# Kernel optimization log

Measured on AMD Instinct MI355X. Metric: run time of the kernel, lower is better.

## Reference

```python
import jax, jax.numpy as jnp
import numpy as np

N = 100_000      # nodes
E = 1_600_000    # edges (no self loops; reference appends them)
G = 1_000        # graphs
FIN = 27         # input node features
HID = 128        # hidden_channels
L = 4            # num_layers
H = 8            # num_heads
B = 4            # num_bases
A = 3            # aggregators: sum, mean, max
FH = HID // H    # per-head out dim
EPS = 1e-5


def setup_inputs() -> dict:
    key = jax.random.key(0)
    ks = jax.random.split(key, 16)
    s = 0.05
    x = jax.random.normal(ks[0], (N, FIN), jnp.float32)
    src = jax.random.randint(ks[1], (E,), 0, N)
    off = jax.random.randint(ks[2], (E,), 1, N)
    dst = (src + off) % N  # guaranteed no self loops
    edge_index = jnp.stack([src, dst]).astype(jnp.int64)
    batch = jnp.sort(jax.random.randint(ks[3], (N,), 0, G)).astype(jnp.int64)
    return {
        "x": x,
        "lin1_w": jax.random.normal(ks[4], (FIN, HID), jnp.float32) * s,
        "lin1_b": jnp.zeros((HID,), jnp.float32),
        "bn1_g": jnp.ones((HID,), jnp.float32),
        "bn1_b": jnp.zeros((HID,), jnp.float32),
        "bases_w": jax.random.normal(ks[5], (L, HID, B * FH), jnp.float32) * s,
        "comb_w": jax.random.normal(ks[6], (L, HID, H * B * A), jnp.float32) * s,
        "comb_b": jnp.zeros((L, H * B * A), jnp.float32),
        "conv_bias": jnp.zeros((L, HID), jnp.float32),
        "bn_g": jnp.ones((L, HID), jnp.float32),
        "bn_b": jnp.zeros((L, HID), jnp.float32),
        "mlp_w1": jax.random.normal(ks[7], (HID, HID // 2), jnp.float32) * s,
        "mbn1_g": jnp.ones((HID // 2,), jnp.float32),
        "mbn1_b": jnp.zeros((HID // 2,), jnp.float32),
        "mlp_w2": jax.random.normal(ks[8], (HID // 2, HID // 4), jnp.float32) * s,
        "mbn2_g": jnp.ones((HID // 4,), jnp.float32),
        "mbn2_b": jnp.zeros((HID // 4,), jnp.float32),
        "mlp_w3": jax.random.normal(ks[9], (HID // 4, 10), jnp.float32) * s,
        "mlp_b3": jnp.zeros((10,), jnp.float32),
        "edge_index": edge_index,
        "batch": batch,
    }


def _bn(h, g, b):
    # BatchNorm1d, training mode (biased batch variance), per-feature over nodes
    mu = jnp.mean(h, axis=0)
    var = jnp.mean((h - mu) ** 2, axis=0)
    return g * (h - mu) * jax.lax.rsqrt(var + EPS) + b


def reference(x, lin1_w, lin1_b, bn1_g, bn1_b, bases_w, comb_w, comb_b,
              conv_bias, bn_g, bn_b, mlp_w1, mbn1_g, mbn1_b, mlp_w2,
              mbn2_g, mbn2_b, mlp_w3, mlp_b3, edge_index, batch):
    # add self loops (inputs contain none, matching remove+add in EGConv)
    loop = jnp.arange(N, dtype=edge_index.dtype)
    src = jnp.concatenate([edge_index[0], loop])
    dst = jnp.concatenate([edge_index[1], loop])

    h = jax.nn.relu(_bn(x @ lin1_w + lin1_b, bn1_g, bn1_b))  # [N, HID]

    ones_e = jnp.ones((src.shape[0], 1), h.dtype)
    deg = jax.ops.segment_sum(ones_e, dst, num_segments=N)  # [N,1], >=1 via self loops

    for l in range(L):
        bases = h @ bases_w[l]                              # [N, B*FH]
        comb = (h @ comb_w[l] + comb_b[l]).reshape(N, H, A * B)
        msg = bases[src]                                    # [E+N, B*FH]
        ssum = jax.ops.segment_sum(msg, dst, num_segments=N)
        smean = ssum / deg
        smax = jax.ops.segment_max(msg, dst, num_segments=N)
        agg = jnp.stack([ssum, smean, smax], axis=1)        # [N, A, B*FH]
        agg = agg.reshape(N, A * B, FH)
        out = jnp.einsum('nhk,nkf->nhf', comb, agg).reshape(N, HID) + conv_bias[l]
        h = h + jax.nn.relu(_bn(out, bn_g[l], bn_b[l]))

    # global mean pool over graphs
    gsum = jax.ops.segment_sum(h, batch, num_segments=G)
    gcnt = jnp.maximum(jax.ops.segment_sum(jnp.ones((N, 1), h.dtype), batch, num_segments=G), 1.0)
    g = gsum / gcnt                                         # [G, HID]

    g = jax.nn.relu(_bn(g @ mlp_w1, mbn1_g, mbn1_b))
    g = jax.nn.relu(_bn(g @ mlp_w2, mbn2_g, mbn2_b))
    return g @ mlp_w3 + mlp_b3                              # [G, 10]
```

## Files before the change

### kernel.cpp

```cpp
#include <hip/hip_runtime.h>

#define EPSV 1e-5f
#define NEGINF -3.402823466e38f
#define NBMAX 1600
#define CHUNK 8192
#define CAP3 6144

typedef short bf16x8 __attribute__((ext_vector_type(8)));
typedef float f32x4 __attribute__((ext_vector_type(4)));

__device__ __forceinline__ unsigned short f2bf(float f) {
    union { float f; unsigned i; } c; c.f = f;
    unsigned r = c.i + 0x7fff + ((c.i >> 16) & 1);
    return (unsigned short)(r >> 16);
}
__device__ __forceinline__ float blo(unsigned u) {
    union { unsigned i; float f; } c; c.i = u << 16; return c.f;
}
__device__ __forceinline__ float bhi(unsigned u) {
    union { unsigned i; float f; } c; c.i = u & 0xffff0000u; return c.f;
}
__device__ __forceinline__ float bfu(unsigned short u) {
    union { unsigned i; float f; } c; c.i = ((unsigned)u) << 16; return c.f;
}

__global__ __launch_bounds__(256)
void k_lin1(const float* __restrict__ x, const float* __restrict__ w,
            const float* __restrict__ bvec, unsigned short* __restrict__ outb,
            float* __restrict__ stats, int N)
{
    __shared__ float wl[27 * 128];
    int tid = threadIdx.x;
    for (int i = tid; i < 27 * 128; i += 256) wl[i] = w[i];
    __syncthreads();

    int l  = tid & 63;
    int wv = tid >> 6;
    float bv0 = bvec[l], bv1 = bvec[64 + l];
    int waveSlots = gridDim.x * 4;
    int trips = (N + waveSlots - 1) / waveSlots;
    float s0 = 0.f, q0 = 0.f, s1 = 0.f, q1 = 0.f;
    for (int it = 0; it < trips; ++it) {
        int n = (it * gridDim.x + blockIdx.x) * 4 + wv;
        if (n < N) {
            const float* xr = x + (size_t)n * 27;
            float a0 = bv0, a1 = bv1;
            #pragma unroll
            for (int k = 0; k < 27; ++k) {
                float xv = xr[k];
                a0 = fmaf(xv, wl[k * 128 + l], a0);
                a1 = fmaf(xv, wl[k * 128 + 64 + l], a1);
            }
            outb[(size_t)n * 128 + l] = f2bf(a0);
            outb[(size_t)n * 128 + 64 + l] = f2bf(a1);
            s0 += a0; q0 += a0 * a0; s1 += a1; q1 += a1 * a1;
        }
    }
    __shared__ float sred[4][256];
    sred[0][tid] = s0; sred[1][tid] = q0;
    sred[2][tid] = s1; sred[3][tid] = q1;
    __syncthreads();
    if (tid < 64) {
        int t = tid;
        float v0 = sred[0][t] + sred[0][t + 64] + sred[0][t + 128] + sred[0][t + 192];
        float v1 = sred[1][t] + sred[1][t + 64] + sred[1][t + 128] + sred[1][t + 192];
        float v2 = sred[2][t] + sred[2][t + 64] + sred[2][t + 128] + sred[2][t + 192];
        float v3 = sred[3][t] + sred[3][t + 64] + sred[3][t + 128] + sred[3][t + 192];
        atomicAdd(stats + t, v0);
        atomicAdd(stats + 128 + t, v1);
        atomicAdd(stats + 64 + t, v2);
        atomicAdd(stats + 192 + t, v3);
    }
}

__global__ __launch_bounds__(256)
void k_prep(const int* __restrict__ dst, int* __restrict__ bcnt, int* __restrict__ bbase,
            int E, int NB, int shift, const int* __restrict__ batch,
            int* __restrict__ gstart, int N, int G, int* __restrict__ arrive)
{
    const int HB = 256;
    int tid = threadIdx.x;
    __shared__ int hist[NBMAX];
    __shared__ int buf2[NBMAX];
    __shared__ int partl[256];
    __shared__ int lastf;

    if (blockIdx.x < HB) {
        for (int i = tid; i < NB; i += 256) hist[i] = 0;
        __syncthreads();
        int stride = HB * 256;
        for (int e = blockIdx.x * 256 + tid; e < E; e += stride)
            atomicAdd(&hist[dst[e] >> shift], 1);
        __syncthreads();
        for (int i = tid; i < NB; i += 256)
            if (hist[i]) atomicAdd(bcnt + i, hist[i]);
        __syncthreads();
        if (tid == 0) {
            __threadfence();
            int tk = atomicAdd(arrive, 1);
            lastf = (tk == HB - 1) ? 1 : 0;
        }
        __syncthreads();
        if (lastf) {
            __threadfence();
            int per = (NB + 255) / 256;
            int beg = tid * per, end = min(beg + per, NB);
            int s = 0;
            for (int i = beg; i < end; ++i) { int v = bcnt[i]; buf2[i] = s; s += v; }
            partl[tid] = s;
            __syncthreads();
            for (int ofs = 1; ofs < 256; ofs <<= 1) {
                int u = (tid >= ofs) ? partl[tid - ofs] : 0;
                __syncthreads();
                partl[tid] += u;
                __syncthreads();
            }
            int add = partl[tid] - s;
            for (int i = beg; i < end; ++i) bbase[i] = buf2[i] + add;
            if (tid == 0) bbase[NB] = E;
        }
    } else {
        int b = blockIdx.x - HB;
        int stride = (gridDim.x - HB) * 256;
        for (int n = b * 256 + tid; n < N; n += stride) {
            int bb = batch[n];
            if (n == 0) {
                for (int g = 0; g <= bb; ++g) gstart[g] = 0;
            } else {
                int pb = batch[n - 1];
                for (int g = pb + 1; g <= bb; ++g) gstart[g] = n;
            }
            if (n == N - 1) {
                for (int g = bb + 1; g <= G; ++g) gstart[g] = N;
            }
        }
    }
}

__global__ __launch_bounds__(256)
void k_p2_scatter(const int* __restrict__ src, const int* __restrict__ dst,
                  const int* __restrict__ bbase, int* __restrict__ bcur0,
                  uint2* __restrict__ bucketed, int E, int NB, int shift)
{
    __shared__ uint2 ebuf[CHUNK];
    __shared__ int hist[NBMAX];
    __shared__ int cur[NBMAX];
    __shared__ int wtmp[256];
    int tid = threadIdx.x;
    int c0 = blockIdx.x * CHUNK;
    int cc = min(CHUNK, E - c0);
    if (cc <= 0) return;

    for (int i = tid; i < NB; i += 256) hist[i] = 0;
    __syncthreads();
    for (int i = tid; i < cc; i += 256)
        atomicAdd(&hist[dst[c0 + i] >> shift], 1);
    __syncthreads();
    int per = (NB + 255) / 256;
    int beg = tid * per, end = min(beg + per, NB);
    int s = 0;
    for (int i = beg; i < end; ++i) s += hist[i];
    wtmp[tid] = s;
    __syncthreads();
    for (int ofs = 1; ofs < 256; ofs <<= 1) {
        int u = (tid >= ofs) ? wtmp[tid - ofs] : 0;
        __syncthreads();
        wtmp[tid] += u;
        __syncthreads();
    }
    int run = wtmp[tid] - s;
    for (int i = beg; i < end; ++i) { cur[i] = run; run += hist[i]; }
    __syncthreads();
    for (int i = tid; i < cc; i += 256) {
        int sv = src[c0 + i], dv = dst[c0 + i];
        int b = dv >> shift;
        int pos = atomicAdd(&cur[b], 1);
        ebuf[pos] = make_uint2((unsigned)sv, (unsigned)dv);
    }
    __syncthreads();
    for (int b = tid; b < NB; b += 256) {
        int c = hist[b];
        if (c > 0) {
            int lb = cur[b] - c;
            int gb = bbase[b] + atomicAdd(&bcur0[b], c);
            hist[b] = gb - lb;
        }
    }
    __syncthreads();
    for (int i = tid; i < cc; i += 256) {
        uint2 u = ebuf[i];
        int b = (int)(u.y >> shift);
        bucketed[hist[b] + i] = u;
    }
}

__global__ __launch_bounds__(256)
void k_p3_csr(const uint2* __restrict__ bucketed, const int* __restrict__ bbase,
              int* __restrict__ rowptr, int* __restrict__ csr,
              int N, int NB, int shift)
{
    __shared__ int ncnt[128], nsc[128];
    __shared__ int lcsr[CAP3];
    int b = blockIdx.x;
    int tid = threadIdx.x;
    int e0 = bbase[b], e1 = bbase[b + 1];
    int cnt = e1 - e0;
    int node0 = b << shift;
    int nodes = min(1 << shift, N - node0);

    if (tid < 128) ncnt[tid] = 0;
    __syncthreads();
    for (int i = tid; i < cnt; i += 256)
        atomicAdd(&ncnt[(int)bucketed[e0 + i].y - node0], 1);
    __syncthreads();
    if (tid < 128) nsc[tid] = ncnt[tid];
    __syncthreads();
    for (int ofs = 1; ofs < 128; ofs <<= 1) {
        int u = 0;
        if (tid < 128 && tid >= ofs) u = nsc[tid - ofs];
        __syncthreads();
        if (tid < 128) nsc[tid] += u;
        __syncthreads();
    }
    if (tid < nodes) rowptr[node0 + tid] = e0 + nsc[tid] - ncnt[tid];
    if (tid == 0 && b == NB - 1) rowptr[N] = e1;
    if (tid < 128) ncnt[tid] = nsc[tid] - ncnt[tid];
    __syncthreads();
    if (cnt <= CAP3) {
        for (int i = tid; i < cnt; i += 256) {
            uint2 u = bucketed[e0 + i];
            int d = (int)u.y - node0;
            int pos = atomicAdd(&ncnt[d], 1);
            lcsr[pos] = (int)u.x;
        }
        __syncthreads();
        for (int i = tid; i < cnt; i += 256) csr[e0 + i] = lcsr[i];
    } else {
        for (int i = tid; i < cnt; i += 256) {
            uint2 u = bucketed[e0 + i];
            int d = (int)u.y - node0;
            int pos = atomicAdd(&ncnt[d], 1);
            csr[e0 + pos] = (int)u.x;
        }
    }
}

__global__ __launch_bounds__(256)
void k_gemm_mfma(const unsigned short* __restrict__ tin, unsigned short* __restrict__ h,
                 const float* __restrict__ stats, const float* __restrict__ gamma,
                 const float* __restrict__ beta, float invN, int residual,
                 const float* __restrict__ basesW, const float* __restrict__ combW,
                 const float* __restrict__ combB,
                 unsigned short* __restrict__ basesP,
                 unsigned short* __restrict__ combB16, int N)
{
    __shared__ unsigned short Wlds[2560 * 8];
    __shared__ float scL[128], shL[128];
    int tid = threadIdx.x;
    if (tid < 128) {
        float mu  = stats[tid] * invN;
        float var = stats[128 + tid] * invN - mu * mu;
        float sc  = gamma[tid] * rsqrtf(var + EPSV);
        scL[tid] = sc;
        shL[tid] = beta[tid] - mu * sc;
    }
    for (int i = tid; i < 2560; i += 256) {
        int ct = i >> 8, rem = i & 255;
        int ln = rem & 63;
        int n16 = ln & 15, quad = ln >> 4;
        int k = ((rem >> 6) << 5) + quad * 8;
        unsigned short tmp[8];
        if (ct < 4) {
            int c = ct * 16 + n16;
            #pragma unroll
            for (int j = 0; j < 8; ++j) tmp[j] = f2bf(basesW[(k + j) * 64 + c]);
        } else {
            int c = (ct - 4) * 16 + n16;
            #pragma unroll
            for (int j = 0; j < 8; ++j) tmp[j] = f2bf(combW[(k + j) * 96 + c]);
        }
        uint4 pk;
        pk.x = (unsigned)tmp[0] | ((unsigned)tmp[1] << 16);
        pk.y = (unsigned)tmp[2] | ((unsigned)tmp[3] << 16);
        pk.z = (unsigned)tmp[4] | ((unsigned)tmp[5] << 16);
        pk.w = (unsigned)tmp[6] | ((unsigned)tmp[7] << 16);
        *(uint4*)&Wlds[(size_t)i * 8] = pk;
    }
    __syncthreads();

    int lane = tid & 63, wv = tid >> 6;
    int f = lane & 15, quad = lane >> 4;
    float cbv[6];
    #pragma unroll
    for (int s = 0; s < 6; ++s) cbv[s] = combB[s * 16 + f];

    int tiles = (N + 15) >> 4;
    int waveSlots = gridDim.x * 4;
    for (int tile = blockIdx.x * 4 + wv; tile < tiles; tile += waveSlots) {
        int tb = tile * 16;
        int mnode = min(tb + f, N - 1);
        size_t rbase = (size_t)mnode * 128;

        f32x4 acc[10];
        #pragma unroll
        for (int ct = 0; ct < 10; ++ct) acc[ct] = (f32x4){0.f, 0.f, 0.f, 0.f};

        #pragma unroll
        for (int ki = 0; ki < 4; ++ki) {
            int kc = quad * 8 + ki * 32;
            uint4 tv = *(const uint4*)&tin[rbase + kc];
            float r0, r1, r2, r3, r4, r5, r6, r7;
            r0 = fmaxf(blo(tv.x) * scL[kc]     + shL[kc],     0.f);
            r1 = fmaxf(bhi(tv.x) * scL[kc + 1] + shL[kc + 1], 0.f);
            r2 = fmaxf(blo(tv.y) * scL[kc + 2] + shL[kc + 2], 0.f);
            r3 = fmaxf(bhi(tv.y) * scL[kc + 3] + shL[kc + 3], 0.f);
            r4 = fmaxf(blo(tv.z) * scL[kc + 4] + shL[kc + 4], 0.f);
            r5 = fmaxf(bhi(tv.z) * scL[kc + 5] + shL[kc + 5], 0.f);
            r6 = fmaxf(blo(tv.w) * scL[kc + 6] + shL[kc + 6], 0.f);
            r7 = fmaxf(bhi(tv.w) * scL[kc + 7] + shL[kc + 7], 0.f);
            if (residual) {
                uint4 hv = *(const uint4*)&h[rbase + kc];
                r0 += blo(hv.x); r1 += bhi(hv.x); r2 += blo(hv.y); r3 += bhi(hv.y);
                r4 += blo(hv.z); r5 += bhi(hv.z); r6 += blo(hv.w); r7 += bhi(hv.w);
            }
            unsigned short b0 = f2bf(r0), b1 = f2bf(r1), b2 = f2bf(r2), b3 = f2bf(r3);
            unsigned short b4 = f2bf(r4), b5 = f2bf(r5), b6 = f2bf(r6), b7 = f2bf(r7);
            uint4 hw;
            hw.x = (unsigned)b0 | ((unsigned)b1 << 16);
            hw.y = (unsigned)b2 | ((unsigned)b3 << 16);
            hw.z = (unsigned)b4 | ((unsigned)b5 << 16);
            hw.w = (unsigned)b6 | ((unsigned)b7 << 16);
            *(uint4*)&h[rbase + kc] = hw;
            short ab[8] = {(short)b0, (short)b1, (short)b2, (short)b3,
                           (short)b4, (short)b5, (short)b6, (short)b7};
            bf16x8 a = *(bf16x8*)ab;
            #pragma unroll
            for (int ct = 0; ct < 10; ++ct) {
                bf16x8 bfr = *(const bf16x8*)&Wlds[(size_t)((ct * 4 + ki) * 64 + lane) * 8];
                acc[ct] = __builtin_amdgcn_mfma_f32_16x16x32_bf16(a, bfr, acc[ct], 0, 0, 0);
            }
        }

        #pragma unroll
        for (int r = 0; r < 4; ++r) {
            int node = tb + quad * 4 + r;
            if (node < N) {
                #pragma unroll
                for (int ct = 0; ct < 4; ++ct)
                    basesP[(size_t)node * 64 + f * 4 + ct] = f2bf(acc[ct][r]);
                #pragma unroll
                for (int s = 0; s < 6; ++s)
                    combB16[(size_t)node * 96 + s * 16 + f] = f2bf(acc[4 + s][r] + cbv[s]);
            }
        }
    }
}

__global__ __launch_bounds__(256)
void k_agg(const unsigned short* __restrict__ basesP, const unsigned short* __restrict__ combB16,
           const int* __restrict__ csr, const int* __restrict__ rowptr,
           const float* __restrict__ cbias, unsigned short* __restrict__ outb,
           float* __restrict__ stats, int N)
{
    int l = threadIdx.x & 63;
    int w = threadIdx.x >> 6;
    int f = l & 15, sub = l >> 4;
    const char* bp = (const char*)basesP;
    unsigned fof = (unsigned)(f << 3);
    float cb0 = cbias[l], cb1 = cbias[64 + l];
    int waveSlots = gridDim.x * 4;
    int pairs = (N + 1) >> 1;
    int trips = (pairs + waveSlots - 1) / waveSlots;
    float s0 = 0.f, q0 = 0.f, s1 = 0.f, q1 = 0.f;

    for (int it = 0; it < trips; ++it) {
        int pr = (it * gridDim.x + blockIdx.x) * 4 + w;
        if (pr < pairs) {
            int nA = pr * 2;
            bool hasB = (nA + 1) < N;
            int nB = hasB ? nA + 1 : nA;
            int rA = rowptr[nA];
            int cA = rowptr[nA + 1] - rA;
            int rB = rowptr[nB];
            int cB = hasB ? (rowptr[nB + 1] - rB) : 0;

            float SA0 = 0.f, SA1 = 0.f, SA2 = 0.f, SA3 = 0.f;
            float MA0 = NEGINF, MA1 = NEGINF, MA2 = NEGINF, MA3 = NEGINF;
            float SB0 = 0.f, SB1 = 0.f, SB2 = 0.f, SB3 = 0.f;
            float MB0 = NEGINF, MB1 = NEGINF, MB2 = NEGINF, MB3 = NEGINF;

            int mt = (max(cA, cB) + 3) >> 2;
            int e = sub;
            #pragma unroll 2
            for (int t = 0; t < mt; ++t) {
                int eA = max(min(e, cA - 1), 0);
                int eB = max(min(e, cB - 1), 0);
                int snA = csr[rA + eA];
                int snB = csr[rB + eB];
                uint2 uA = *(const uint2*)(bp + (((unsigned)snA) << 7) + fof);
                uint2 uB = *(const uint2*)(bp + (((unsigned)snB) << 7) + fof);
                bool vA = e < cA, vB = e < cB;
                float a0 = blo(uA.x), a1 = bhi(uA.x), a2 = blo(uA.y), a3 = bhi(uA.y);
                float b0 = blo(uB.x), b1 = bhi(uB.x), b2 = blo(uB.y), b3 = bhi(uB.y);
                SA0 += vA ? a0 : 0.f; SA1 += vA ? a1 : 0.f;
                SA2 += vA ? a2 : 0.f; SA3 += vA ? a3 : 0.f;
                MA0 = fmaxf(MA0, vA ? a0 : NEGINF); MA1 = fmaxf(MA1, vA ? a1 : NEGINF);
                MA2 = fmaxf(MA2, vA ? a2 : NEGINF); MA3 = fmaxf(MA3, vA ? a3 : NEGINF);
                SB0 += vB ? b0 : 0.f; SB1 += vB ? b1 : 0.f;
                SB2 += vB ? b2 : 0.f; SB3 += vB ? b3 : 0.f;
                MB0 = fmaxf(MB0, vB ? b0 : NEGINF); MB1 = fmaxf(MB1, vB ? b1 : NEGINF);
                MB2 = fmaxf(MB2, vB ? b2 : NEGINF); MB3 = fmaxf(MB3, vB ? b3 : NEGINF);
                e += 4;
            }

            #pragma unroll
            for (int m = 0; m < 2; ++m) {
                if (m == 1 && !hasB) break;
                int n = (m == 0) ? nA : nB;
                int cnt = (m == 0) ? cA : cB;
                float T0 = (m == 0) ? SA0 : SB0, T1 = (m == 0) ? SA1 : SB1;
                float T2 = (m == 0) ? SA2 : SB2, T3 = (m == 0) ? SA3 : SB3;
                float X0 = (m == 0) ? MA0 : MB0, X1 = (m == 0) ? MA1 : MB1;
                float X2 = (m == 0) ? MA2 : MB2, X3 = (m == 0) ? MA3 : MB3;
                T0 += __shfl_xor(T0, 16, 64); T1 += __shfl_xor(T1, 16, 64);
                T2 += __shfl_xor(T2, 16, 64); T3 += __shfl_xor(T3, 16, 64);
                T0 += __shfl_xor(T0, 32, 64); T1 += __shfl_xor(T1, 32, 64);
                T2 += __shfl_xor(T2, 32, 64); T3 += __shfl_xor(T3, 32, 64);
                X0 = fmaxf(X0, __shfl_xor(X0, 16, 64)); X1 = fmaxf(X1, __shfl_xor(X1, 16, 64));
                X2 = fmaxf(X2, __shfl_xor(X2, 16, 64)); X3 = fmaxf(X3, __shfl_xor(X3, 16, 64));
                X0 = fmaxf(X0, __shfl_xor(X0, 32, 64)); X1 = fmaxf(X1, __shfl_xor(X1, 32, 64));
                X2 = fmaxf(X2, __shfl_xor(X2, 32, 64)); X3 = fmaxf(X3, __shfl_xor(X3, 32, 64));
                uint2 su = *(const uint2*)(bp + (((unsigned)n) << 7) + fof);
                float w0 = blo(su.x), w1 = bhi(su.x), w2 = blo(su.y), w3 = bhi(su.y);
                T0 += w0; T1 += w1; T2 += w2; T3 += w3;
                X0 = fmaxf(X0, w0); X1 = fmaxf(X1, w1);
                X2 = fmaxf(X2, w2); X3 = fmaxf(X3, w3);
                float invd = 1.f / (float)(cnt + 1);
                float A0 = T0 * invd, A1 = T1 * invd, A2 = T2 * invd, A3 = T3 * invd;

                const unsigned short* cr = combB16 + (size_t)n * 96;
                const uint2* c0p = (const uint2*)(cr + sub * 12);
                const uint2* c1p = (const uint2*)(cr + 48 + sub * 12);
                uint2 qa0 = c0p[0], qa1 = c0p[1], qa2 = c0p[2];
                uint2 qb0 = c1p[0], qb1 = c1p[1], qb2 = c1p[2];

                float o0 = cb0, o1 = cb1;
                o0 = fmaf(blo(qa0.x), T0, o0); o0 = fmaf(bhi(qa0.x), T1, o0);
                o0 = fmaf(blo(qa0.y), T2, o0); o0 = fmaf(bhi(qa0.y), T3, o0);
                o0 = fmaf(blo(qa1.x), A0, o0); o0 = fmaf(bhi(qa1.x), A1, o0);
                o0 = fmaf(blo(qa1.y), A2, o0); o0 = fmaf(bhi(qa1.y), A3, o0);
                o0 = fmaf(blo(qa2.x), X0, o0); o0 = fmaf(bhi(qa2.x), X1, o0);
                o0 = fmaf(blo(qa2.y), X2, o0); o0 = fmaf(bhi(qa2.y), X3, o0);
                o1 = fmaf(blo(qb0.x), T0, o1); o1 = fmaf(bhi(qb0.x), T1, o1);
                o1 = fmaf(blo(qb0.y), T2, o1); o1 = fmaf(bhi(qb0.y), T3, o1);
                o1 = fmaf(blo(qb1.x), A0, o1); o1 = fmaf(bhi(qb1.x), A1, o1);
                o1 = fmaf(blo(qb1.y), A2, o1); o1 = fmaf(bhi(qb1.y), A3, o1);
                o1 = fmaf(blo(qb2.x), X0, o1); o1 = fmaf(bhi(qb2.x), X1, o1);
                o1 = fmaf(blo(qb2.y), X2, o1); o1 = fmaf(bhi(qb2.y), X3, o1);

                outb[(size_t)n * 128 + l] = f2bf(o0);
                outb[(size_t)n * 128 + 64 + l] = f2bf(o1);
                s0 += o0; q0 += o0 * o0; s1 += o1; q1 += o1 * o1;
            }
        }
    }
    __shared__ float sred[4][256];
    sred[0][threadIdx.x] = s0; sred[1][threadIdx.x] = q0;
    sred[2][threadIdx.x] = s1; sred[3][threadIdx.x] = q1;
    __syncthreads();
    if (threadIdx.x < 64) {
        int t = threadIdx.x;
        float v0 = sred[0][t] + sred[0][t + 64] + sred[0][t + 128] + sred[0][t + 192];
        float v1 = sred[1][t] + sred[1][t + 64] + sred[1][t + 128] + sred[1][t + 192];
        float v2 = sred[2][t] + sred[2][t + 64] + sred[2][t + 128] + sred[2][t + 192];
        float v3 = sred[3][t] + sred[3][t + 64] + sred[3][t + 128] + sred[3][t + 192];
        atomicAdd(stats + t, v0);
        atomicAdd(stats + 128 + t, v1);
        atomicAdd(stats + 64 + t, v2);
        atomicAdd(stats + 192 + t, v3);
    }
}

__global__ __launch_bounds__(256)
void k_gmean(const unsigned short* __restrict__ t, const unsigned short* __restrict__ h,
             const float* __restrict__ stats, const float* __restrict__ gamma,
             const float* __restrict__ beta, float invN,
             const int* __restrict__ gstart, float* __restrict__ gout, int G)
{
    __shared__ float part[128];
    int g = blockIdx.x;
    if (g >= G) return;
    int c = threadIdx.x & 127;
    int half = threadIdx.x >> 7;
    float mu  = stats[c] * invN;
    float var = stats[128 + c] * invN - mu * mu;
    float sc  = gamma[c] * rsqrtf(var + EPSV);
    float sh  = beta[c] - mu * sc;
    int s = gstart[g], e = gstart[g + 1];
    float acc = 0.f;
    #pragma unroll 2
    for (int n = s + half; n < e; n += 2) {
        size_t o = (size_t)n * 128 + c;
        acc += bfu(h[o]) + fmaxf(bfu(t[o]) * sc + sh, 0.f);
    }
    if (half) part[c] = acc;
    __syncthreads();
    if (!half) {
        float tot = acc + part[c];
        float cntf = fmaxf((float)(e - s), 1.f);
        gout[g * 128 + c] = tot / cntf;
    }
}

__global__ void k_mlp1(const float* __restrict__ gin, const float* __restrict__ w1,
                       float* __restrict__ t1, float* __restrict__ stats, int G)
{
    int g = blockIdx.x;
    int c = threadIdx.x;
    const float* gr = gin + g * 128;
    float acc = 0.f;
    for (int k = 0; k < 128; ++k) acc = fmaf(gr[k], w1[k * 64 + c], acc);
    t1[g * 64 + c] = acc;
    atomicAdd(stats + c, acc);
    atomicAdd(stats + 64 + c, acc * acc);
}

__global__ void k_mlp2(const float* __restrict__ t1, const float* __restrict__ stats1,
                       const float* __restrict__ g1, const float* __restrict__ b1,
                       const float* __restrict__ w2, float* __restrict__ t2,
                       float* __restrict__ stats2, float invG, int G)
{
    __shared__ float row[64];
    int g = blockIdx.x;
    int c = threadIdx.x;
    float v = t1[g * 64 + c];
    float mu = stats1[c] * invG;
    float var = stats1[64 + c] * invG - mu * mu;
    row[c] = fmaxf(g1[c] * (v - mu) * rsqrtf(var + EPSV) + b1[c], 0.f);
    __syncthreads();
    if (c < 32) {
        float acc = 0.f;
        #pragma unroll
        for (int k = 0; k < 64; ++k) acc = fmaf(row[k], w2[k * 32 + c], acc);
        t2[g * 32 + c] = acc;
        atomicAdd(stats2 + c, acc);
        atomicAdd(stats2 + 32 + c, acc * acc);
    }
}

__global__ void k_mlp3(const float* __restrict__ t2, const float* __restrict__ stats2,
                       const float* __restrict__ g2, const float* __restrict__ b2,
                       const float* __restrict__ w3, const float* __restrict__ b3,
                       float* __restrict__ out, float invG, int G)
{
    __shared__ float row[32];
    int g = blockIdx.x;
    int c = threadIdx.x;
    if (c < 32) {
        float v = t2[g * 32 + c];
        float mu = stats2[c] * invG;
        float var = stats2[32 + c] * invG - mu * mu;
        row[c] = fmaxf(g2[c] * (v - mu) * rsqrtf(var + EPSV) + b2[c], 0.f);
    }
    __syncthreads();
    if (c < 10) {
        float acc = b3[c];
        #pragma unroll
        for (int k = 0; k < 32; ++k) acc = fmaf(row[k], w3[k * 10 + c], acc);
        out[g * 10 + c] = acc;
    }
}

extern "C" void kernel_launch(void* const* d_in, const int* in_sizes, int n_in,
                              void* d_out, int out_size, void* d_ws, size_t ws_size,
                              hipStream_t stream)
{
    const float* x        = (const float*)d_in[0];
    const float* lin1_w   = (const float*)d_in[1];
    const float* lin1_b   = (const float*)d_in[2];
    const float* bn1_g    = (const float*)d_in[3];
    const float* bn1_b    = (const float*)d_in[4];
    const float* bases_w  = (const float*)d_in[5];
    const float* comb_w   = (const float*)d_in[6];
    const float* comb_b   = (const float*)d_in[7];
    const float* conv_bias= (const float*)d_in[8];
    const float* bn_g     = (const float*)d_in[9];
    const float* bn_b     = (const float*)d_in[10];
    const float* mlp_w1   = (const float*)d_in[11];
    const float* mbn1_g   = (const float*)d_in[12];
    const float* mbn1_b   = (const float*)d_in[13];
    const float* mlp_w2   = (const float*)d_in[14];
    const float* mbn2_g   = (const float*)d_in[15];
    const float* mbn2_b   = (const float*)d_in[16];
    const float* mlp_w3   = (const float*)d_in[17];
    const float* mlp_b3   = (const float*)d_in[18];
    const int*   edge_idx = (const int*)d_in[19];
    const int*   batch    = (const int*)d_in[20];
    float* outp = (float*)d_out;

    const int N = in_sizes[20];
    const int E = in_sizes[19] / 2;
    const int G = out_size / 10;
    const int* esrc = edge_idx;
    const int* edst = edge_idx + E;

    int shift = 6;
    while ((((N - 1) >> shift) + 1) > NBMAX && shift < 7) ++shift;
    const int NB = ((N - 1) >> shift) + 1;

    char* p = (char*)d_ws;
    auto alloc = [&](size_t bytes) {
        char* r = p;
        p += (bytes + 255) & ~(size_t)255;
        return r;
    };
    unsigned short* h      = (unsigned short*)alloc((size_t)N * 128 * 2);
    unsigned short* basesP = (unsigned short*)alloc((size_t)N * 64 * 2);
    unsigned short* combB16= (unsigned short*)alloc((size_t)N * 96 * 2);
    unsigned short* outb   = (unsigned short*)alloc((size_t)N * 128 * 2);
    int*            csr    = (int*)  alloc((size_t)(E + 64) * 4);
    int*            rowptr = (int*)  alloc((size_t)(N + 1) * 4);
    int*            bbase  = (int*)  alloc((size_t)(NB + 1) * 4);
    float*          tg     = (float*)alloc((size_t)G * 128 * 4);
    float*          t1     = (float*)alloc((size_t)G * 64 * 4);
    float*          t2     = (float*)alloc((size_t)G * 32 * 4);
    int*            gstart = (int*)  alloc((size_t)(G + 1) * 4);
    char*           zbase  = p;
    int*            bcnt   = (int*)  alloc((size_t)NB * 4);
    int*            bcur0  = (int*)  alloc((size_t)NB * 4);
    float*          stats  = (float*)alloc(7 * 256 * 4);
    int*            arrive = (int*)  alloc(2 * 4);
    size_t zbytes = (size_t)(p - zbase);
    uint2* bucketed = (uint2*)combB16;
    (void)ws_size; (void)n_in;

    hipMemsetAsync(zbase, 0, zbytes, stream);

    const float invN = 1.0f / (float)N;
    const float invG = 1.0f / (float)G;

    k_lin1<<<1024, 256, 0, stream>>>(x, lin1_w, lin1_b, outb, stats, N);
    k_prep<<<768, 256, 0, stream>>>(edst, bcnt, bbase, E, NB, shift,
                                    batch, gstart, N, G, arrive);
    k_p2_scatter<<<(E + CHUNK - 1) / CHUNK, 256, 0, stream>>>(esrc, edst, bbase, bcur0,
                                                              bucketed, E, NB, shift);
    k_p3_csr<<<NB, 256, 0, stream>>>(bucketed, bbase, rowptr, csr, N, NB, shift);

    for (int l = 0; l < 4; ++l) {
        const float* bw = bases_w + (size_t)l * 128 * 64;
        const float* cw = comb_w + (size_t)l * 128 * 96;
        const float* cb = comb_b + (size_t)l * 96;
        const float* cvb = conv_bias + (size_t)l * 128;
        const float* pg = (l == 0) ? bn1_g : bn_g + (l - 1) * 128;
        const float* pb = (l == 0) ? bn1_b : bn_b + (l - 1) * 128;
        k_gemm_mfma<<<1024, 256, 0, stream>>>(outb, h, stats + l * 256, pg, pb, invN,
                                              l > 0 ? 1 : 0, bw, cw, cb, basesP, combB16, N);
        k_agg<<<2048, 256, 0, stream>>>(basesP, combB16, csr, rowptr, cvb,
                                        outb, stats + (1 + l) * 256, N);
    }

    k_gmean<<<G, 256, 0, stream>>>(outb, h, stats + 4 * 256, bn_g + 3 * 128,
                                   bn_b + 3 * 128, invN, gstart, tg, G);
    float* st5 = stats + 5 * 256;
    float* st6 = stats + 6 * 256;
    k_mlp1<<<G, 64, 0, stream>>>(tg, mlp_w1, t1, st5, G);
    k_mlp2<<<G, 64, 0, stream>>>(t1, st5, mbn1_g, mbn1_b, mlp_w2, t2, st6, invG, G);
    k_mlp3<<<G, 64, 0, stream>>>(t2, st6, mbn2_g, mbn2_b, mlp_w3, mlp_b3, outp, invG, G);
}
```

Measured before the change: 816.6 us.

## Fuse pooling with first MLP layer, pack bases stores, retune grids

Merges the global mean pool kernel and the first MLP matmul into one kernel, so the pooled graph features stay in shared memory and one launch plus one round trip are dropped. The four bf16 stores per node for bases become a single packed 8-byte store. It also halves the scatter CHUNK size, which doubles the scatter grid, and halves the GEMM grid to 512 blocks. These several unrelated tweaks change the balance between parallelism and per-block work in different kernels.

```diff
diff --git a/kernel.cpp b/kernel.cpp
--- a/kernel.cpp
+++ b/kernel.cpp
@@ -3,7 +3,7 @@
 #define EPSV 1e-5f
 #define NEGINF -3.402823466e38f
 #define NBMAX 1600
-#define CHUNK 8192
+#define CHUNK 4096
 #define CAP3 6144
 
 typedef short bf16x8 __attribute__((ext_vector_type(8)));
@@ -345,9 +345,10 @@
         for (int r = 0; r < 4; ++r) {
             int node = tb + quad * 4 + r;
             if (node < N) {
-                #pragma unroll
-                for (int ct = 0; ct < 4; ++ct)
-                    basesP[(size_t)node * 64 + f * 4 + ct] = f2bf(acc[ct][r]);
+                uint2 bpk;
+                bpk.x = (unsigned)f2bf(acc[0][r]) | ((unsigned)f2bf(acc[1][r]) << 16);
+                bpk.y = (unsigned)f2bf(acc[2][r]) | ((unsigned)f2bf(acc[3][r]) << 16);
+                *(uint2*)&basesP[(size_t)node * 64 + f * 4] = bpk;
                 #pragma unroll
                 for (int s = 0; s < 6; ++s)
                     combB16[(size_t)node * 96 + s * 16 + f] = f2bf(acc[4 + s][r] + cbv[s]);
@@ -482,47 +483,52 @@
 }
 
 __global__ __launch_bounds__(256)
-void k_gmean(const unsigned short* __restrict__ t, const unsigned short* __restrict__ h,
-             const float* __restrict__ stats, const float* __restrict__ gamma,
-             const float* __restrict__ beta, float invN,
-             const int* __restrict__ gstart, float* __restrict__ gout, int G)
-{
+void k_pool(const unsigned short* __restrict__ t, const unsigned short* __restrict__ h,
+            const float* __restrict__ stats, const float* __restrict__ gamma,
+            const float* __restrict__ beta, float invN, const int* __restrict__ gstart,
+            const float* __restrict__ w1, float* __restrict__ t1,
+            float* __restrict__ st5, int G)
+{
+    __shared__ float tg[128];
     __shared__ float part[128];
+    __shared__ float red[4][64];
     int g = blockIdx.x;
     if (g >= G) return;
-    int c = threadIdx.x & 127;
-    int half = threadIdx.x >> 7;
-    float mu  = stats[c] * invN;
-    float var = stats[128 + c] * invN - mu * mu;
-    float sc  = gamma[c] * rsqrtf(var + EPSV);
-    float sh  = beta[c] - mu * sc;
-    int s = gstart[g], e = gstart[g + 1];
-    float acc = 0.f;
-    #pragma unroll 2
-    for (int n = s + half; n < e; n += 2) {
-        size_t o = (size_t)n * 128 + c;
-        acc += bfu(h[o]) + fmaxf(bfu(t[o]) * sc + sh, 0.f);
-    }
-    if (half) part[c] = acc;
-    __syncthreads();
-    if (!half) {
-        float tot = acc + part[c];
-        float cntf = fmaxf((float)(e - s), 1.f);
-        gout[g * 128 + c] = tot / cntf;
-    }
-}
-
-__global__ void k_mlp1(const float* __restrict__ gin, const float* __restrict__ w1,
-                       float* __restrict__ t1, float* __restrict__ stats, int G)
-{
-    int g = blockIdx.x;
-    int c = threadIdx.x;
-    const float* gr = gin + g * 128;
-    float acc = 0.f;
-    for (int k = 0; k < 128; ++k) acc = fmaf(gr[k], w1[k * 64 + c], acc);
-    t1[g * 64 + c] = acc;
-    atomicAdd(stats + c, acc);
-    atomicAdd(stats + 64 + c, acc * acc);
+    int tid = threadIdx.x;
+    {
+        int c = tid & 127, half = tid >> 7;
+        float mu  = stats[c] * invN;
+        float var = stats[128 + c] * invN - mu * mu;
+        float sc  = gamma[c] * rsqrtf(var + EPSV);
+        float sh  = beta[c] - mu * sc;
+        int s = gstart[g], e = gstart[g + 1];
+        float acc = 0.f;
+        #pragma unroll 2
+        for (int n = s + half; n < e; n += 2) {
+            size_t o = (size_t)n * 128 + c;
+            acc += bfu(h[o]) + fmaxf(bfu(t[o]) * sc + sh, 0.f);
+        }
+        if (half) part[c] = acc;
+        __syncthreads();
+        if (!half) tg[c] = (acc + part[c]) / fmaxf((float)(e - s), 1.f);
+        __syncthreads();
+    }
+    {
+        int cc = tid & 63, pp = tid >> 6;
+        float a = 0.f;
+        int k0 = pp * 32;
+        #pragma unroll
+        for (int k = 0; k < 32; ++k)
+            a = fmaf(tg[k0 + k], w1[(k0 + k) * 64 + cc], a);
+        red[pp][cc] = a;
+        __syncthreads();
+        if (tid < 64) {
+            float v = red[0][tid] + red[1][tid] + red[2][tid] + red[3][tid];
+            t1[g * 64 + tid] = v;
+            atomicAdd(st5 + tid, v);
+            atomicAdd(st5 + 64 + tid, v * v);
+        }
+    }
 }
 
 __global__ void k_mlp2(const float* __restrict__ t1, const float* __restrict__ stats1,
@@ -621,7 +627,6 @@
     int*            csr    = (int*)  alloc((size_t)(E + 64) * 4);
     int*            rowptr = (int*)  alloc((size_t)(N + 1) * 4);
     int*            bbase  = (int*)  alloc((size_t)(NB + 1) * 4);
-    float*          tg     = (float*)alloc((size_t)G * 128 * 4);
     float*          t1     = (float*)alloc((size_t)G * 64 * 4);
     float*          t2     = (float*)alloc((size_t)G * 32 * 4);
     int*            gstart = (int*)  alloc((size_t)(G + 1) * 4);
@@ -653,17 +658,17 @@
         const float* cvb = conv_bias + (size_t)l * 128;
         const float* pg = (l == 0) ? bn1_g : bn_g + (l - 1) * 128;
         const float* pb = (l == 0) ? bn1_b : bn_b + (l - 1) * 128;
-        k_gemm_mfma<<<1024, 256, 0, stream>>>(outb, h, stats + l * 256, pg, pb, invN,
-                                              l > 0 ? 1 : 0, bw, cw, cb, basesP, combB16, N);
+        k_gemm_mfma<<<512, 256, 0, stream>>>(outb, h, stats + l * 256, pg, pb, invN,
+                                             l > 0 ? 1 : 0, bw, cw, cb, basesP, combB16, N);
         k_agg<<<2048, 256, 0, stream>>>(basesP, combB16, csr, rowptr, cvb,
                                         outb, stats + (1 + l) * 256, N);
     }
 
-    k_gmean<<<G, 256, 0, stream>>>(outb, h, stats + 4 * 256, bn_g + 3 * 128,
-                                   bn_b + 3 * 128, invN, gstart, tg, G);
+    k_pool<<<G, 256, 0, stream>>>(outb, h, stats + 4 * 256, bn_g + 3 * 128,
+                                  bn_b + 3 * 128, invN, gstart,
+                                  mlp_w1, t1, stats + 5 * 256, G);
     float* st5 = stats + 5 * 256;
     float* st6 = stats + 6 * 256;
-    k_mlp1<<<G, 64, 0, stream>>>(tg, mlp_w1, t1, st5, G);
     k_mlp2<<<G, 64, 0, stream>>>(t1, st5, mbn1_g, mbn1_b, mlp_w2, t2, st6, invG, G);
     k_mlp3<<<G, 64, 0, stream>>>(t2, st6, mbn2_g, mbn2_b, mlp_w3, mlp_b3, outp, invG, G);
 }
```

After: 771.3 us. 5.6% less time.
